# Kernel tuning notes

Hardware: AMD Instinct MI355X
Metric: run time of the kernel (lower is better)

The kernel has to match this reference:

```python
import jax, jax.numpy as jnp
import numpy as np

MEM = 128   # mem_dim
K = 4096    # number of object keys (each an array leaf list)
L = 128     # numbers per array
STATS_CAP = 100  # number_stats list capped at 100 entries


def setup_inputs() -> dict:
    key = jax.random.key(0)
    ks = jax.random.split(key, 13)
    s = 0.05
    return {
        "numbers": jax.random.normal(ks[0], (K, L), jnp.float32),
        "w_num": jax.random.normal(ks[1], (MEM,), jnp.float32) * s,
        "b_num": jax.random.normal(ks[2], (MEM,), jnp.float32) * s,
        "W_ih": jax.random.normal(ks[3], (4 * MEM, 2 * MEM), jnp.float32) * s,
        "W_hh": jax.random.normal(ks[4], (4 * MEM, MEM), jnp.float32) * s,
        "b_ih": jax.random.normal(ks[5], (4 * MEM,), jnp.float32) * s,
        "b_hh": jax.random.normal(ks[6], (4 * MEM,), jnp.float32) * s,
        "W_fh": jax.random.normal(ks[7], (MEM, MEM), jnp.float32) * s,
        "b_fh": jax.random.normal(ks[8], (MEM,), jnp.float32) * s,
        "W_iouh": jax.random.normal(ks[9], (3 * MEM, MEM), jnp.float32) * s,
        "b_iouh": jax.random.normal(ks[10], (3 * MEM,), jnp.float32) * s,
        "W_lout": jax.random.normal(ks[11], (MEM, MEM), jnp.float32) * s,
        "b_lout": jax.random.normal(ks[12], (MEM,), jnp.float32) * s,
    }


def _normalize_numbers(x_flat):
    # Replicates embed_number's running number_stats (tie_primitives -> one shared
    # '___default___' stats list, filled in traversal order, capped at 100 entries).
    # The k-th number is normalized by mean/std over the first min(k, 100) numbers
    # (including itself); std division only when len > 3 and std not ~0.
    n = x_flat.shape[0]
    k = jnp.arange(1, n + 1, dtype=jnp.float32)
    cs = jnp.cumsum(x_flat)
    css = jnp.cumsum(x_flat * x_flat)
    cap = jnp.minimum(k, float(STATS_CAP))
    cs_c = jnp.where(k <= STATS_CAP, cs, cs[STATS_CAP - 1])
    css_c = jnp.where(k <= STATS_CAP, css, css[STATS_CAP - 1])
    mean = cs_c / cap
    var = jnp.maximum(css_c / cap - mean * mean, 0.0)
    std = jnp.sqrt(var)
    # torch impl computes stats with numpy -> no gradient flows through them
    mean = jax.lax.stop_gradient(mean)
    std = jax.lax.stop_gradient(std)
    y = x_flat - mean
    use_std = (cap > 3.0) & (std > 1e-8)
    return jnp.where(use_std, y / jnp.where(use_std, std, 1.0), y)


def _forward(numbers, w_num, b_num, W_ih, W_hh, b_ih, b_hh,
             W_fh, b_fh, W_iouh, b_iouh, W_lout, b_lout):
    # --- embed_number: per-leaf (c=0, h = Linear(1, MEM)(norm_num)) ---
    x = _normalize_numbers(numbers.reshape(-1)).reshape(K, L)
    h_num = x[..., None] * w_num + b_num  # [K, L, MEM]

    # --- embed_array: LSTMCell over each array's children; input = cat([c_child, h_child]) ---
    # child_c is always 0 for number leaves.
    def step(carry, h_t):  # h_t: [K, MEM]
        c, h = carry
        xcat = jnp.concatenate([jnp.zeros_like(h_t), h_t], axis=-1)  # [K, 2*MEM]
        gates = xcat @ W_ih.T + b_ih + h @ W_hh.T + b_hh             # [K, 4*MEM]
        i, f, g, o = jnp.split(gates, 4, axis=-1)
        c2 = jax.nn.sigmoid(f) * c + jax.nn.sigmoid(i) * jnp.tanh(g)
        h2 = jax.nn.sigmoid(o) * jnp.tanh(c2)
        return (c2, h2), None

    z = jnp.zeros((K, MEM), numbers.dtype)
    (c_arr, h_arr), _ = jax.lax.scan(step, (z, z), jnp.swapaxes(h_num, 0, 1))
    # c_arr, h_arr: [K, MEM] final states per array child of the root object

    # --- embed_object (root): child-sum Tree-LSTM gating ---
    f_g = jax.nn.sigmoid(h_arr @ W_fh.T + b_fh)             # [K, MEM]
    fc_sum = jnp.sum(f_g * c_arr, axis=0, keepdims=True)    # [1, MEM]
    hs_bar = jnp.sum(h_arr, axis=0, keepdims=True)          # [1, MEM]
    iou = hs_bar @ W_iouh.T + b_iouh
    i, o, u = jnp.split(iou, 3, axis=-1)
    c = jax.nn.sigmoid(i) * jnp.tanh(u) + fc_sum
    h = jax.nn.sigmoid(o) * jnp.tanh(c)
    h_hat = h @ W_lout.T + b_lout
    return jnp.concatenate([c, h_hat], axis=1)  # [1, 2*MEM]


def reference(numbers, w_num, b_num, W_ih, W_hh, b_ih, b_hh,
              W_fh, b_fh, W_iouh, b_iouh, W_lout, b_lout):
    return _forward(numbers, w_num, b_num, W_ih, W_hh, b_ih, b_hh,
                    W_fh, b_fh, W_iouh, b_iouh, W_lout, b_lout)
```

## Files before the change

### kernel.cpp

```cpp
#include <hip/hip_runtime.h>
#include <math.h>

#define L2E 1.4426950408889634f
#define HSTR 136

typedef __bf16 bf16x8 __attribute__((ext_vector_type(8)));
typedef float  f32x4  __attribute__((ext_vector_type(4)));

__device__ __forceinline__ float sig2(float y) {
    return __builtin_amdgcn_rcpf(1.0f + __builtin_amdgcn_exp2f(-y));
}

__global__ __launch_bounds__(1024, 4) void lstm_kernel(
        const float* __restrict__ numbers,
        const float* __restrict__ w_num, const float* __restrict__ b_num,
        const float* __restrict__ W_ih,  const float* __restrict__ W_hh,
        const float* __restrict__ b_ih,  const float* __restrict__ b_hh,
        const float* __restrict__ W_fh,  const float* __restrict__ b_fh,
        float* __restrict__ partials) {
    __shared__ unsigned short hbuf[2][16 * HSTR];
    __shared__ float xls[128 * 16];
    __shared__ float abw[8 * 128];
    __shared__ float wnum_s[128], bnum_s[128];
    __shared__ float sx[100], lutm[100], luti[100];
    __shared__ float accs[256];
    __shared__ float s_m99, s_i99;

    const int tid  = threadIdx.x;
    const int lane = tid & 63;
    const int wave = tid >> 6;
    const int par  = wave >> 3;
    const int quad = lane >> 4;
    const int lcol = lane & 15;
    const int m0   = (wave & 7) * 16;
    const int r0   = blockIdx.x * 16;

    if (tid < 128) { wnum_s[tid] = w_num[tid]; bnum_s[tid] = b_num[tid]; }
    if (tid < 100) sx[tid] = numbers[tid];
    if (tid < 256) accs[tid] = 0.0f;
    for (int i = tid; i < 16 * HSTR; i += 1024) hbuf[0][i] = 0;
    __syncthreads();

    if (wave == 0) {
        float v1 = sx[lane];
        float v2 = (lane < 36) ? sx[64 + lane] : 0.0f;
        float s = v1 + v2, ss = v1 * v1 + v2 * v2;
        #pragma unroll
        for (int off = 32; off >= 1; off >>= 1) {
            s += __shfl_xor(s, off);
            ss += __shfl_xor(ss, off);
        }
        if (lane == 0) {
            float mean = s * 0.01f;
            float var  = ss * 0.01f - mean * mean;
            if (var < 0.f) var = 0.f;
            float sd = sqrtf(var);
            s_m99 = mean;
            s_i99 = (sd > 1e-8f) ? (1.0f / sd) : 1.0f;
        }
    }
    if (blockIdx.x == 0 && tid < 100) {
        float s = 0.f, ss = 0.f;
        for (int j = 0; j <= tid; ++j) { float v = sx[j]; s += v; ss += v * v; }
        float cap  = (float)(tid + 1);
        float mean = s / cap;
        float var  = ss / cap - mean * mean;
        if (var < 0.f) var = 0.f;
        float sd = sqrtf(var);
        lutm[tid] = mean;
        luti[tid] = (cap > 3.0f && sd > 1e-8f) ? (1.0f / sd) : 1.0f;
    }
    {
        int g = lane >> 4;
        int j = g * 128 + m0 + lcol;
        const float* row = W_ih + j * 256 + 128;
        float a = 0.f, b = 0.f;
        #pragma unroll 4
        for (int m = 0; m < 128; m += 4) {
            f32x4 w  = *(const f32x4*)(row + m);
            f32x4 wn = *(const f32x4*)(wnum_s + m);
            f32x4 bn = *(const f32x4*)(bnum_s + m);
            a += w[0]*wn[0] + w[1]*wn[1] + w[2]*wn[2] + w[3]*wn[3];
            b += w[0]*bn[0] + w[1]*bn[1] + w[2]*bn[2] + w[3]*bn[3];
        }
        float sc = (g == 2) ? (2.0f * L2E) : L2E;
        abw[(wave & 7) * 128 + lane]      = a * sc;
        abw[(wave & 7) * 128 + 64 + lane] = (b + b_ih[j] + b_hh[j]) * sc;
    }
    __syncthreads();

    for (int i = tid; i < 2048; i += 1024) {
        int row = i >> 7, t = i & 127;
        int flat = (r0 + row) * 128 + t;
        float v = numbers[flat];
        float mn, iv;
        if (flat < 100) { mn = lutm[flat]; iv = luti[flat]; }
        else            { mn = s_m99;     iv = s_i99; }
        xls[t * 16 + row] = (v - mn) * iv;
    }

    bf16x8 bfr[4][4];
    #pragma unroll
    for (int g = 0; g < 4; ++g) {
        float sc = (g == 2) ? (2.0f * L2E) : L2E;
        #pragma unroll
        for (int kk = 0; kk < 4; ++kk) {
            const float* p = W_hh + (g * 128 + m0 + lcol) * 128 + kk * 32 + quad * 8;
            f32x4 w0 = *(const f32x4*)p;
            f32x4 w1 = *(const f32x4*)(p + 4);
            bf16x8 bt;
            #pragma unroll
            for (int q = 0; q < 4; ++q) {
                bt[q]     = (__bf16)(w0[q] * sc);
                bt[q + 4] = (__bf16)(w1[q] * sc);
            }
            bfr[g][kk] = bt;
        }
    }
    float ag[4], bg[4];
    #pragma unroll
    for (int g = 0; g < 4; ++g) {
        ag[g] = abw[(wave & 7) * 128 + g * 16 + lcol];
        bg[g] = abw[(wave & 7) * 128 + 64 + g * 16 + lcol];
    }
    float c0 = 0.f, c1 = 0.f, h0 = 0.f, h1 = 0.f;
    __syncthreads();

#define ROW_TAIL(R, cS, hS)                                                          \
    {                                                                                \
        float e1 = __builtin_amdgcn_exp2f(-aI[R]);                                   \
        float e2 = __builtin_amdgcn_exp2f(aG[R]);                                    \
        float pp = (e2 - 1.0f) * __builtin_amdgcn_rcpf((1.0f + e1) * (e2 + 1.0f));   \
        float sf = sig2(aF[R]);                                                      \
        float cn = sf * cS + pp;                                                     \
        cS = cn;                                                                     \
        float e3 = __builtin_amdgcn_exp2f(cn * (2.0f * L2E));                        \
        float e4 = __builtin_amdgcn_exp2f(-aO[R]);                                   \
        hS = (e3 - 1.0f) * __builtin_amdgcn_rcpf((1.0f + e4) * (e3 + 1.0f));         \
        hout[(quad * 4 + (R)) * HSTR + m0 + lcol] =                                  \
            __builtin_bit_cast(unsigned short, (__bf16)hS);                          \
    }

    for (int t = 0; t < 128; ++t) {
        const unsigned short* hin  = hbuf[t & 1];
        unsigned short*       hout = hbuf[(t + 1) & 1];
        f32x4 xq = *(const f32x4*)(const void*)(xls + t * 16 + quad * 4);
        f32x4 aI, aG, aF, aO;
        #pragma unroll
        for (int r = 0; r < 4; ++r) {
            aI[r] = xq[r] * ag[0] + bg[0];
            aF[r] = xq[r] * ag[1] + bg[1];
            aG[r] = xq[r] * ag[2] + bg[2];
            aO[r] = xq[r] * ag[3] + bg[3];
        }
        #pragma unroll
        for (int kk = 0; kk < 4; ++kk) {
            bf16x8 af = *(const bf16x8*)(const void*)(hin + lcol * HSTR + kk * 32 + quad * 8);
            aI = __builtin_amdgcn_mfma_f32_16x16x32_bf16(af, bfr[0][kk], aI, 0, 0, 0);
            aF = __builtin_amdgcn_mfma_f32_16x16x32_bf16(af, bfr[1][kk], aF, 0, 0, 0);
            aG = __builtin_amdgcn_mfma_f32_16x16x32_bf16(af, bfr[2][kk], aG, 0, 0, 0);
            aO = __builtin_amdgcn_mfma_f32_16x16x32_bf16(af, bfr[3][kk], aO, 0, 0, 0);
        }
        if (par == 0) {
            ROW_TAIL(0, c0, h0)
            ROW_TAIL(1, c1, h1)
        } else {
            ROW_TAIL(2, c0, h0)
            ROW_TAIL(3, c1, h1)
        }
        __syncthreads();
    }
#undef ROW_TAIL

    {
        float v = h0 + h1;
        v += __shfl_xor(v, 16);
        v += __shfl_xor(v, 32);
        if (lane < 16) atomicAdd(&accs[m0 + lane], v);
    }
    {
        f32x4 facc;
        float bb = b_fh[m0 + lcol] * L2E;
        #pragma unroll
        for (int r = 0; r < 4; ++r) facc[r] = bb;
        #pragma unroll
        for (int kk = 0; kk < 4; ++kk) {
            bf16x8 afr = *(const bf16x8*)(const void*)(hbuf[0] + lcol * HSTR + kk * 32 + quad * 8);
            const float* p = W_fh + (m0 + lcol) * 128 + kk * 32 + quad * 8;
            f32x4 w0 = *(const f32x4*)p;
            f32x4 w1 = *(const f32x4*)(p + 4);
            bf16x8 wt;
            #pragma unroll
            for (int q = 0; q < 4; ++q) {
                wt[q]     = (__bf16)(w0[q] * L2E);
                wt[q + 4] = (__bf16)(w1[q] * L2E);
            }
            facc = __builtin_amdgcn_mfma_f32_16x16x32_bf16(afr, wt, facc, 0, 0, 0);
        }
        float fcv = (par == 0) ? (sig2(facc[0]) * c0 + sig2(facc[1]) * c1)
                               : (sig2(facc[2]) * c0 + sig2(facc[3]) * c1);
        fcv += __shfl_xor(fcv, 16);
        fcv += __shfl_xor(fcv, 32);
        if (lane < 16) atomicAdd(&accs[128 + m0 + lane], fcv);
    }
    __syncthreads();
    if (tid < 256) partials[blockIdx.x * 256 + tid] = accs[tid];
}

__global__ void finalize_kernel(const float* __restrict__ partials,
                                const float* __restrict__ W_iouh,
                                const float* __restrict__ b_iouh,
                                const float* __restrict__ W_lout,
                                const float* __restrict__ b_lout,
                                float* __restrict__ out) {
    __shared__ float hsb[128], fcs[128], iou[384], hfin[128];
    int tid = threadIdx.x;
    if (tid < 256) {
        int m = tid & 127, sel = tid >> 7;
        const float* p = partials + sel * 128 + m;
        float s0 = 0.f, s1 = 0.f, s2 = 0.f, s3 = 0.f;
        #pragma unroll 4
        for (int b = 0; b < 256; b += 4) {
            s0 += p[(b + 0) * 256];
            s1 += p[(b + 1) * 256];
            s2 += p[(b + 2) * 256];
            s3 += p[(b + 3) * 256];
        }
        float s = (s0 + s1) + (s2 + s3);
        if (sel == 0) hsb[m] = s; else fcs[m] = s;
    }
    __syncthreads();
    if (tid < 384) {
        float s = b_iouh[tid];
        const f32x4* row = (const f32x4*)(W_iouh + tid * 128);
        #pragma unroll 8
        for (int m = 0; m < 32; ++m) {
            f32x4 w = row[m];
            s += w[0]*hsb[4*m] + w[1]*hsb[4*m+1] + w[2]*hsb[4*m+2] + w[3]*hsb[4*m+3];
        }
        iou[tid] = s;
    }
    __syncthreads();
    if (tid < 128) {
        float i = iou[tid], o = iou[128 + tid], u = iou[256 + tid];
        float cf = sig2(i * L2E) * (2.0f * sig2(u * 2.0f * L2E) - 1.0f) + fcs[tid];
        out[tid] = cf;
        hfin[tid] = sig2(o * L2E) * (2.0f * sig2(cf * 2.0f * L2E) - 1.0f);
    }
    __syncthreads();
    if (tid < 128) {
        float s = b_lout[tid];
        const f32x4* row = (const f32x4*)(W_lout + tid * 128);
        #pragma unroll 8
        for (int m = 0; m < 32; ++m) {
            f32x4 w = row[m];
            s += w[0]*hfin[4*m] + w[1]*hfin[4*m+1] + w[2]*hfin[4*m+2] + w[3]*hfin[4*m+3];
        }
        out[128 + tid] = s;
    }
}

extern "C" void kernel_launch(void* const* d_in, const int* in_sizes, int n_in,
                              void* d_out, int out_size, void* d_ws, size_t ws_size,
                              hipStream_t stream) {
    const float* numbers = (const float*)d_in[0];
    const float* w_num   = (const float*)d_in[1];
    const float* b_num   = (const float*)d_in[2];
    const float* W_ih    = (const float*)d_in[3];
    const float* W_hh    = (const float*)d_in[4];
    const float* b_ih    = (const float*)d_in[5];
    const float* b_hh    = (const float*)d_in[6];
    const float* W_fh    = (const float*)d_in[7];
    const float* b_fh    = (const float*)d_in[8];
    const float* W_iouh  = (const float*)d_in[9];
    const float* b_iouh  = (const float*)d_in[10];
    const float* W_lout  = (const float*)d_in[11];
    const float* b_lout  = (const float*)d_in[12];
    float* out = (float*)d_out;

    float* partials = (float*)d_ws;

    lstm_kernel<<<256, 1024, 0, stream>>>(numbers, w_num, b_num, W_ih, W_hh,
                                          b_ih, b_hh, W_fh, b_fh, partials);
    finalize_kernel<<<1, 384, 0, stream>>>(partials, W_iouh, b_iouh, W_lout, b_lout, out);
}
```

Before: 264.3 us.

## Halve block size, give each wave all 4 rows, fuse finalize via last-block flag

The block drops from 1024 to 512 threads, so each wave now runs the gate tail for all four MFMA output rows instead of splitting rows across two wave halves. The forget-gate sigmoid is folded into a shared reciprocal, the time loop is unrolled by two to avoid buffer indexing, and the h sum is read back from the final bf16 buffer. The separate finalize kernel is replaced by a last-block-done atomic counter, with a memset added to reset the counter each launch. This trades a kernel launch and some sync width for more serial transcendental work per wave in the recurrent loop.

Result: faster. 236.6 us (-10.5%).

```diff
diff --git a/kernel.cpp b/kernel.cpp
--- a/kernel.cpp
+++ b/kernel.cpp
@@ -1,7 +1,8 @@
 #include <hip/hip_runtime.h>
 #include <math.h>
 
-#define L2E 1.4426950408889634f
+#define L2E  1.4426950408889634f
+#define TL2E 2.8853900817779268f
 #define HSTR 136
 
 typedef __bf16 bf16x8 __attribute__((ext_vector_type(8)));
@@ -11,34 +12,37 @@
     return __builtin_amdgcn_rcpf(1.0f + __builtin_amdgcn_exp2f(-y));
 }
 
-__global__ __launch_bounds__(1024, 4) void lstm_kernel(
+__global__ __launch_bounds__(512, 2) void lstm_kernel(
         const float* __restrict__ numbers,
         const float* __restrict__ w_num, const float* __restrict__ b_num,
         const float* __restrict__ W_ih,  const float* __restrict__ W_hh,
         const float* __restrict__ b_ih,  const float* __restrict__ b_hh,
         const float* __restrict__ W_fh,  const float* __restrict__ b_fh,
-        float* __restrict__ partials) {
+        const float* __restrict__ W_iouh, const float* __restrict__ b_iouh,
+        const float* __restrict__ W_lout, const float* __restrict__ b_lout,
+        float* __restrict__ partials, int* __restrict__ flag,
+        float* __restrict__ out) {
     __shared__ unsigned short hbuf[2][16 * HSTR];
     __shared__ float xls[128 * 16];
-    __shared__ float abw[8 * 128];
-    __shared__ float wnum_s[128], bnum_s[128];
+    __shared__ float abw[1024];
+    __shared__ float wnb[256];
     __shared__ float sx[100], lutm[100], luti[100];
-    __shared__ float accs[256];
+    __shared__ float fin[768];
     __shared__ float s_m99, s_i99;
+    __shared__ int s_last;
 
     const int tid  = threadIdx.x;
     const int lane = tid & 63;
     const int wave = tid >> 6;
-    const int par  = wave >> 3;
     const int quad = lane >> 4;
     const int lcol = lane & 15;
-    const int m0   = (wave & 7) * 16;
+    const int m0   = wave * 16;
     const int r0   = blockIdx.x * 16;
 
-    if (tid < 128) { wnum_s[tid] = w_num[tid]; bnum_s[tid] = b_num[tid]; }
+    if (tid < 128) wnb[tid] = w_num[tid];
+    else if (tid < 256) wnb[tid] = b_num[tid - 128];
     if (tid < 100) sx[tid] = numbers[tid];
-    if (tid < 256) accs[tid] = 0.0f;
-    for (int i = tid; i < 16 * HSTR; i += 1024) hbuf[0][i] = 0;
+    for (int i = tid; i < 16 * HSTR; i += 512) hbuf[0][i] = 0;
     __syncthreads();
 
     if (wave == 0) {
@@ -71,25 +75,24 @@
         luti[tid] = (cap > 3.0f && sd > 1e-8f) ? (1.0f / sd) : 1.0f;
     }
     {
-        int g = lane >> 4;
-        int j = g * 128 + m0 + lcol;
+        int j = tid;
         const float* row = W_ih + j * 256 + 128;
         float a = 0.f, b = 0.f;
         #pragma unroll 4
         for (int m = 0; m < 128; m += 4) {
             f32x4 w  = *(const f32x4*)(row + m);
-            f32x4 wn = *(const f32x4*)(wnum_s + m);
-            f32x4 bn = *(const f32x4*)(bnum_s + m);
+            f32x4 wn = *(const f32x4*)(wnb + m);
+            f32x4 bn = *(const f32x4*)(wnb + 128 + m);
             a += w[0]*wn[0] + w[1]*wn[1] + w[2]*wn[2] + w[3]*wn[3];
             b += w[0]*bn[0] + w[1]*bn[1] + w[2]*bn[2] + w[3]*bn[3];
         }
-        float sc = (g == 2) ? (2.0f * L2E) : L2E;
-        abw[(wave & 7) * 128 + lane]      = a * sc;
-        abw[(wave & 7) * 128 + 64 + lane] = (b + b_ih[j] + b_hh[j]) * sc;
-    }
-    __syncthreads();
-
-    for (int i = tid; i < 2048; i += 1024) {
+        float sc = (j >= 256 && j < 384) ? TL2E : L2E;
+        abw[j]       = a * sc;
+        abw[512 + j] = (b + b_ih[j] + b_hh[j]) * sc;
+    }
+    __syncthreads();
+
+    for (int i = tid; i < 2048; i += 512) {
         int row = i >> 7, t = i & 127;
         int flat = (r0 + row) * 128 + t;
         float v = numbers[flat];
@@ -102,7 +105,7 @@
     bf16x8 bfr[4][4];
     #pragma unroll
     for (int g = 0; g < 4; ++g) {
-        float sc = (g == 2) ? (2.0f * L2E) : L2E;
+        float sc = (g == 2) ? TL2E : L2E;
         #pragma unroll
         for (int kk = 0; kk < 4; ++kk) {
             const float* p = W_hh + (g * 128 + m0 + lcol) * 128 + kk * 32 + quad * 8;
@@ -120,32 +123,20 @@
     float ag[4], bg[4];
     #pragma unroll
     for (int g = 0; g < 4; ++g) {
-        ag[g] = abw[(wave & 7) * 128 + g * 16 + lcol];
-        bg[g] = abw[(wave & 7) * 128 + 64 + g * 16 + lcol];
-    }
-    float c0 = 0.f, c1 = 0.f, h0 = 0.f, h1 = 0.f;
-    __syncthreads();
-
-#define ROW_TAIL(R, cS, hS)                                                          \
-    {                                                                                \
-        float e1 = __builtin_amdgcn_exp2f(-aI[R]);                                   \
-        float e2 = __builtin_amdgcn_exp2f(aG[R]);                                    \
-        float pp = (e2 - 1.0f) * __builtin_amdgcn_rcpf((1.0f + e1) * (e2 + 1.0f));   \
-        float sf = sig2(aF[R]);                                                      \
-        float cn = sf * cS + pp;                                                     \
-        cS = cn;                                                                     \
-        float e3 = __builtin_amdgcn_exp2f(cn * (2.0f * L2E));                        \
-        float e4 = __builtin_amdgcn_exp2f(-aO[R]);                                   \
-        hS = (e3 - 1.0f) * __builtin_amdgcn_rcpf((1.0f + e4) * (e3 + 1.0f));         \
-        hout[(quad * 4 + (R)) * HSTR + m0 + lcol] =                                  \
-            __builtin_bit_cast(unsigned short, (__bf16)hS);                          \
-    }
-
-    for (int t = 0; t < 128; ++t) {
-        const unsigned short* hin  = hbuf[t & 1];
-        unsigned short*       hout = hbuf[(t + 1) & 1];
+        ag[g] = abw[g * 128 + m0 + lcol];
+        bg[g] = abw[512 + g * 128 + m0 + lcol];
+    }
+    float cst[4] = {0.f, 0.f, 0.f, 0.f};
+    __syncthreads();
+
+    auto step = [&](int t, const unsigned short* hinb, unsigned short* houtb) {
+        const unsigned short* hp = hinb + lcol * HSTR + quad * 8;
+        bf16x8 af[4];
+        #pragma unroll
+        for (int kk = 0; kk < 4; ++kk)
+            af[kk] = *(const bf16x8*)(const void*)(hp + kk * 32);
         f32x4 xq = *(const f32x4*)(const void*)(xls + t * 16 + quad * 4);
-        f32x4 aI, aG, aF, aO;
+        f32x4 aI, aF, aG, aO;
         #pragma unroll
         for (int r = 0; r < 4; ++r) {
             aI[r] = xq[r] * ag[0] + bg[0];
@@ -155,28 +146,43 @@
         }
         #pragma unroll
         for (int kk = 0; kk < 4; ++kk) {
-            bf16x8 af = *(const bf16x8*)(const void*)(hin + lcol * HSTR + kk * 32 + quad * 8);
-            aI = __builtin_amdgcn_mfma_f32_16x16x32_bf16(af, bfr[0][kk], aI, 0, 0, 0);
-            aF = __builtin_amdgcn_mfma_f32_16x16x32_bf16(af, bfr[1][kk], aF, 0, 0, 0);
-            aG = __builtin_amdgcn_mfma_f32_16x16x32_bf16(af, bfr[2][kk], aG, 0, 0, 0);
-            aO = __builtin_amdgcn_mfma_f32_16x16x32_bf16(af, bfr[3][kk], aO, 0, 0, 0);
-        }
-        if (par == 0) {
-            ROW_TAIL(0, c0, h0)
-            ROW_TAIL(1, c1, h1)
-        } else {
-            ROW_TAIL(2, c0, h0)
-            ROW_TAIL(3, c1, h1)
+            aI = __builtin_amdgcn_mfma_f32_16x16x32_bf16(af[kk], bfr[0][kk], aI, 0, 0, 0);
+            aF = __builtin_amdgcn_mfma_f32_16x16x32_bf16(af[kk], bfr[1][kk], aF, 0, 0, 0);
+            aG = __builtin_amdgcn_mfma_f32_16x16x32_bf16(af[kk], bfr[2][kk], aG, 0, 0, 0);
+            aO = __builtin_amdgcn_mfma_f32_16x16x32_bf16(af[kk], bfr[3][kk], aO, 0, 0, 0);
+        }
+        unsigned short* wp = houtb + quad * 4 * HSTR + m0 + lcol;
+        #pragma unroll
+        for (int r = 0; r < 4; ++r) {
+            float e1 = __builtin_amdgcn_exp2f(-aI[r]);
+            float e2 = __builtin_amdgcn_exp2f(aG[r]);
+            float e5 = __builtin_amdgcn_exp2f(-aF[r]);
+            float D1 = (1.0f + e1) * (e2 + 1.0f);
+            float D2 = 1.0f + e5;
+            float R  = __builtin_amdgcn_rcpf(D1 * D2);
+            float c2 = (cst[r] * D1 + (e2 - 1.0f) * D2) * R;
+            cst[r] = c2;
+            float e3 = __builtin_amdgcn_exp2f(c2 * TL2E);
+            float e4 = __builtin_amdgcn_exp2f(-aO[r]);
+            float R2 = __builtin_amdgcn_rcpf((1.0f + e4) * (e3 + 1.0f));
+            float h  = (e3 - 1.0f) * R2;
+            wp[r * HSTR] = __builtin_bit_cast(unsigned short, (__bf16)h);
         }
         __syncthreads();
-    }
-#undef ROW_TAIL
-
-    {
-        float v = h0 + h1;
-        v += __shfl_xor(v, 16);
-        v += __shfl_xor(v, 32);
-        if (lane < 16) atomicAdd(&accs[m0 + lane], v);
+    };
+    for (int t = 0; t < 128; t += 2) {
+        step(t,     hbuf[0], hbuf[1]);
+        step(t + 1, hbuf[1], hbuf[0]);
+    }
+
+    {
+        float hv = 0.f;
+        #pragma unroll
+        for (int r = 0; r < 4; ++r)
+            hv += (float)__builtin_bit_cast(__bf16, hbuf[0][(quad * 4 + r) * HSTR + m0 + lcol]);
+        hv += __shfl_xor(hv, 16);
+        hv += __shfl_xor(hv, 32);
+        if (lane < 16) partials[blockIdx.x * 256 + m0 + lane] = hv;
     }
     {
         f32x4 facc;
@@ -197,37 +203,37 @@
             }
             facc = __builtin_amdgcn_mfma_f32_16x16x32_bf16(afr, wt, facc, 0, 0, 0);
         }
-        float fcv = (par == 0) ? (sig2(facc[0]) * c0 + sig2(facc[1]) * c1)
-                               : (sig2(facc[2]) * c0 + sig2(facc[3]) * c1);
+        float fcv = 0.f;
+        #pragma unroll
+        for (int r = 0; r < 4; ++r) fcv += sig2(facc[r]) * cst[r];
         fcv += __shfl_xor(fcv, 16);
         fcv += __shfl_xor(fcv, 32);
-        if (lane < 16) atomicAdd(&accs[128 + m0 + lane], fcv);
-    }
-    __syncthreads();
-    if (tid < 256) partials[blockIdx.x * 256 + tid] = accs[tid];
-}
-
-__global__ void finalize_kernel(const float* __restrict__ partials,
-                                const float* __restrict__ W_iouh,
-                                const float* __restrict__ b_iouh,
-                                const float* __restrict__ W_lout,
-                                const float* __restrict__ b_lout,
-                                float* __restrict__ out) {
-    __shared__ float hsb[128], fcs[128], iou[384], hfin[128];
-    int tid = threadIdx.x;
-    if (tid < 256) {
-        int m = tid & 127, sel = tid >> 7;
-        const float* p = partials + sel * 128 + m;
+        if (lane < 16) partials[blockIdx.x * 256 + 128 + m0 + lane] = fcv;
+    }
+
+    __threadfence();
+    __syncthreads();
+    if (tid == 0) s_last = atomicAdd(flag, 1);
+    __syncthreads();
+    if (s_last != 255) return;
+    __threadfence();
+
+    {
+        int j = tid & 255;
+        int half = tid >> 8;
+        const float* p = partials + half * 128 * 256 + j;
         float s0 = 0.f, s1 = 0.f, s2 = 0.f, s3 = 0.f;
-        #pragma unroll 4
-        for (int b = 0; b < 256; b += 4) {
+        #pragma unroll 2
+        for (int b = 0; b < 128; b += 4) {
             s0 += p[(b + 0) * 256];
             s1 += p[(b + 1) * 256];
             s2 += p[(b + 2) * 256];
             s3 += p[(b + 3) * 256];
         }
         float s = (s0 + s1) + (s2 + s3);
-        if (sel == 0) hsb[m] = s; else fcs[m] = s;
+        if (half == 0) fin[j] = s;
+        __syncthreads();
+        if (half == 1) fin[j] += s;
     }
     __syncthreads();
     if (tid < 384) {
@@ -236,16 +242,16 @@
         #pragma unroll 8
         for (int m = 0; m < 32; ++m) {
             f32x4 w = row[m];
-            s += w[0]*hsb[4*m] + w[1]*hsb[4*m+1] + w[2]*hsb[4*m+2] + w[3]*hsb[4*m+3];
-        }
-        iou[tid] = s;
+            s += w[0]*fin[4*m] + w[1]*fin[4*m+1] + w[2]*fin[4*m+2] + w[3]*fin[4*m+3];
+        }
+        fin[256 + tid] = s;
     }
     __syncthreads();
     if (tid < 128) {
-        float i = iou[tid], o = iou[128 + tid], u = iou[256 + tid];
-        float cf = sig2(i * L2E) * (2.0f * sig2(u * 2.0f * L2E) - 1.0f) + fcs[tid];
+        float i = fin[256 + tid], o = fin[384 + tid], u = fin[512 + tid];
+        float cf = sig2(i * L2E) * (2.0f * sig2(u * TL2E) - 1.0f) + fin[128 + tid];
         out[tid] = cf;
-        hfin[tid] = sig2(o * L2E) * (2.0f * sig2(cf * 2.0f * L2E) - 1.0f);
+        fin[640 + tid] = sig2(o * L2E) * (2.0f * sig2(cf * TL2E) - 1.0f);
     }
     __syncthreads();
     if (tid < 128) {
@@ -254,7 +260,7 @@
         #pragma unroll 8
         for (int m = 0; m < 32; ++m) {
             f32x4 w = row[m];
-            s += w[0]*hfin[4*m] + w[1]*hfin[4*m+1] + w[2]*hfin[4*m+2] + w[3]*hfin[4*m+3];
+            s += w[0]*fin[640+4*m] + w[1]*fin[641+4*m] + w[2]*fin[642+4*m] + w[3]*fin[643+4*m];
         }
         out[128 + tid] = s;
     }
@@ -279,8 +285,11 @@
     float* out = (float*)d_out;
 
     float* partials = (float*)d_ws;
-
-    lstm_kernel<<<256, 1024, 0, stream>>>(numbers, w_num, b_num, W_ih, W_hh,
-                                          b_ih, b_hh, W_fh, b_fh, partials);
-    finalize_kernel<<<1, 384, 0, stream>>>(partials, W_iouh, b_iouh, W_lout, b_lout, out);
+    int*   flag     = (int*)((float*)d_ws + 256 * 256);
+
+    hipMemsetAsync(flag, 0, sizeof(int), stream);
+    lstm_kernel<<<256, 512, 0, stream>>>(numbers, w_num, b_num, W_ih, W_hh,
+                                         b_ih, b_hh, W_fh, b_fh,
+                                         W_iouh, b_iouh, W_lout, b_lout,
+                                         partials, flag, out);
 }
```
